# Kernel optimization log

Hardware: AMD Instinct MI355X
Metric: run time of the kernel (lower is better)

## Reference

```python
import jax, jax.numpy as jnp
import numpy as np

DIMS = 4

def mlp(x, W1, b1, W2, b2, W3, b3, Wo, bo):
    # x: (4,) -> scalar log(g_rr)
    h = jnp.tanh(x @ W1 + b1)
    h = jnp.tanh(h @ W2 + b2)
    h = jnp.tanh(h @ W3 + b3)
    return (h @ Wo + bo)[0]

def metric(x, params):
    # build_g: spherical metric with learned g_rr = exp(net(x))
    g_rr = jnp.exp(mlp(x, *params))
    r, th = x[1], x[2]
    diag = jnp.stack([-jnp.ones(()), g_rr, r ** 2, (r * jnp.sin(th)) ** 2])
    return jnp.diag(diag)  # (4,4)

def christoffel(x, params):
    g = metric(x, params)
    dg = jax.jacfwd(lambda xx: metric(xx, params))(x)  # dg[i,j,k] = d g_ij / d x^k
    g_inv = jnp.linalg.inv(g)
    # Gamma^a_bc = 0.5 g^{ad} (d_c g_db + d_b g_dc - d_d g_bc)
    sym = dg + jnp.transpose(dg, (0, 2, 1)) - jnp.transpose(dg, (2, 0, 1))
    gamma = 0.5 * jnp.einsum('ad,dbc->abc', g_inv, sym)
    return gamma, g_inv

def einstein_per_sample(x, params):
    gamma, g_inv = christoffel(x, params)
    # D[a,i,j,k] = d_k Gamma^a_ij (second nested forward-mode jacobian)
    D = jax.jacfwd(lambda xx: christoffel(xx, params)[0])(x)
    # R^a_bcd = d_c Gamma^a_db - d_d Gamma^a_cb + G^a_ce G^e_db - G^a_de G^e_cb
    riemann = (jnp.einsum('adbc->abcd', D) - jnp.einsum('acbd->abcd', D)
               + jnp.einsum('ace,edb->abcd', gamma, gamma)
               - jnp.einsum('ade,ecb->abcd', gamma, gamma))
    ricci = jnp.einsum('abad->bd', riemann)
    ricci_scalar = jnp.einsum('bd,bd->', g_inv, ricci)
    ricci_up = jnp.einsum('ac,bd,cd->ab', g_inv, g_inv, ricci)
    return ricci_up - 0.5 * g_inv * ricci_scalar  # contravariant Einstein tensor


def setup_inputs() -> dict:
    key = jax.random.key(0)
    ks = jax.random.split(key, 5)
    B, H = 8192, 256
    # coords in a well-conditioned region (avoid r ~ 0 which makes g singular)
    coords = jax.random.uniform(ks[0], (B, DIMS), dtype=jnp.float32) * 0.9 + 0.1
    def w(k, shape):
        fan_in = shape[0]
        return jax.random.normal(k, shape, dtype=jnp.float32) / np.sqrt(fan_in)
    return {
        'coords': coords,
        'W1': w(ks[1], (DIMS, H)), 'b1': jnp.zeros((H,), jnp.float32),
        'W2': w(ks[2], (H, H)),   'b2': jnp.zeros((H,), jnp.float32),
        'W3': w(ks[3], (H, H)),   'b3': jnp.zeros((H,), jnp.float32),
        'Wo': w(ks[4], (H, 1)),   'bo': jnp.zeros((1,), jnp.float32),
    }


def reference(coords, W1, b1, W2, b2, W3, b3, Wo, bo):
    params = (W1, b1, W2, b2, W3, b3, Wo, bo)
    # Batched Einstein tensor G^{ab}(x) for every sample: (B, 4, 4)
    return jax.vmap(lambda x: einstein_per_sample(x, params))(coords)
```

## Files before the change

### kernel.cpp

```cpp
#include <hip/hip_runtime.h>
#include <math.h>

typedef _Float16 half8 __attribute__((ext_vector_type(8)));
typedef float floatx4 __attribute__((ext_vector_type(4)));

#define HDIM 256
#define NC 15
#define NCP 16
#define SPB 8
#define MR 128
#define NWAVE 4
#define NT 4


__device__ __forceinline__ void einstein_tail(
    float f, const float* Gf, const float* Hs, float r, float th,
    float* __restrict__ outp)
{
    float Hf[4][4];
    {
        int qq = 0;
#pragma unroll
        for (int k = 0; k < 4; ++k)
#pragma unroll
            for (int l = k; l < 4; ++l) { Hf[k][l] = Hs[qq]; Hf[l][k] = Hs[qq]; ++qq; }
    }
    float sn = sinf(th), cs = cosf(th);
    float E  = expf(f);

    float gd[4] = {-1.f, E, r * r, r * r * sn * sn};
    float gi[4];
#pragma unroll
    for (int a = 0; a < 4; ++a) gi[a] = 1.f / gd[a];

    float dgv[4][4];
    float ddg[4][4][4];
#pragma unroll
    for (int a = 0; a < 4; ++a)
#pragma unroll
        for (int k = 0; k < 4; ++k) {
            dgv[a][k] = 0.f;
#pragma unroll
            for (int l = 0; l < 4; ++l) ddg[a][k][l] = 0.f;
        }
#pragma unroll
    for (int k = 0; k < 4; ++k) dgv[1][k] = E * Gf[k];
    dgv[2][1] = 2.f * r;
    dgv[3][1] = 2.f * r * sn * sn;
    dgv[3][2] = 2.f * r * r * sn * cs;
#pragma unroll
    for (int k = 0; k < 4; ++k)
#pragma unroll
        for (int l = 0; l < 4; ++l)
            ddg[1][k][l] = E * fmaf(Gf[k], Gf[l], Hf[k][l]);
    ddg[2][1][1] = 2.f;
    ddg[3][1][1] = 2.f * sn * sn;
    ddg[3][1][2] = 4.f * r * sn * cs;
    ddg[3][2][1] = 4.f * r * sn * cs;
    ddg[3][2][2] = 2.f * r * r * (cs * cs - sn * sn);

    auto SYMF = [&](int a, int i, int jx) -> float {
        float sy = 0.f;
        if (a == i)  sy += dgv[a][jx];
        if (a == jx) sy += dgv[a][i];
        if (i == jx) sy -= dgv[i][a];
        return sy;
    };
    auto DF = [&](int a, int i, int jx, int k) -> float {
        float ds = 0.f;
        if (a == i)  ds += ddg[a][jx][k];
        if (a == jx) ds += ddg[a][i][k];
        if (i == jx) ds -= ddg[i][a][k];
        return 0.5f * (gi[a] * ds - gi[a] * gi[a] * dgv[a][k] * SYMF(a, i, jx));
    };

    float Gm[4][4][4];
#pragma unroll
    for (int a = 0; a < 4; ++a)
#pragma unroll
        for (int i = 0; i < 4; ++i)
#pragma unroll
            for (int jx = 0; jx < 4; ++jx)
                Gm[a][i][jx] = 0.5f * gi[a] * SYMF(a, i, jx);

    float ric[4][4];
#pragma unroll
    for (int b = 0; b < 4; ++b)
#pragma unroll
        for (int d = 0; d < 4; ++d) {
            float sum = 0.f;
#pragma unroll
            for (int a = 0; a < 4; ++a) {
                sum += DF(a, d, b, a) - DF(a, a, b, d);
#pragma unroll
                for (int e = 0; e < 4; ++e)
                    sum += Gm[a][a][e] * Gm[e][d][b] - Gm[a][d][e] * Gm[e][a][b];
            }
            ric[b][d] = sum;
        }

    float Rs = 0.f;
#pragma unroll
    for (int b = 0; b < 4; ++b) Rs += gi[b] * ric[b][b];

#pragma unroll
    for (int a = 0; a < 4; ++a)
#pragma unroll
        for (int b = 0; b < 4; ++b) {
            float v = gi[a] * gi[b] * ric[a][b];
            if (a == b) v -= 0.5f * gi[a] * Rs;
            outp[a * 4 + b] = v;
        }
}

__global__ __launch_bounds__(256) void pack_wt(
    const float* __restrict__ W2, const float* __restrict__ W3,
    _Float16* __restrict__ Wt)
{
    __shared__ float t[64][65];
    const int m    = blockIdx.x >> 4;
    const float* W = m ? W3 : W2;
    const int tile = blockIdx.x & 15;
    const int k0 = (tile >> 2) * 64, j0 = (tile & 3) * 64;
    const int tx = threadIdx.x & 63, ty = threadIdx.x >> 6;
#pragma unroll
    for (int i = 0; i < 16; ++i) {
        int k = ty + i * 4;
        t[k][tx] = W[(k0 + k) * HDIM + j0 + tx];
    }
    __syncthreads();
#pragma unroll
    for (int i = 0; i < 16; ++i) {
        int jj = ty + i * 4;
        Wt[(size_t)m * HDIM * HDIM + (j0 + jj) * HDIM + k0 + tx] =
            (_Float16)t[tx][jj];
    }
}

template <bool TW>
__global__ __launch_bounds__(256, 2) void mlp_fused(
    const float* __restrict__ coords,
    const float* __restrict__ W1, const float* __restrict__ b1,
    const float* __restrict__ W2, const float* __restrict__ b2,
    const float* __restrict__ W3, const float* __restrict__ b3,
    const float* __restrict__ Wo, const float* __restrict__ bo,
    const _Float16* __restrict__ Wt,
    float* __restrict__ out, int B)
{
    __shared__ __align__(16) _Float16 st[MR * HDIM];

    const int tid  = threadIdx.x;
    const int w    = tid >> 6;
    const int lane = tid & 63;
    const int col  = lane & 15;
    const int q    = lane >> 4;
    const int s0   = blockIdx.x * SPB;

    floatx4 acc[8][NT];

    auto f4get = [](const float4& v, int i) -> float {
        switch (i & 3) { case 0: return v.x; case 1: return v.y;
                         case 2: return v.z; default: return v.w; }
    };

    auto produce1 = [&]() {
        const int sl = tid & 7;
        const int tc = tid >> 3;
        int ss = s0 + sl; if (ss >= B) ss = B - 1;
        const float x0 = coords[ss * 4 + 0];
        const float x1 = coords[ss * 4 + 1];
        const float x2 = coords[ss * 4 + 2];
        const float x3 = coords[ss * 4 + 3];
        const int jg = tc * 8;
        float4 wa[4][2];
#pragma unroll
        for (int k = 0; k < 4; ++k) {
            wa[k][0] = *(const float4*)&W1[k * HDIM + jg];
            wa[k][1] = *(const float4*)&W1[k * HDIM + jg + 4];
        }
        float4 bb0 = *(const float4*)&b1[jg];
        float4 bb1 = *(const float4*)&b1[jg + 4];
        half8 ch[NCP];
#pragma unroll
        for (int jj = 0; jj < 8; ++jj) ch[15][jj] = (_Float16)0.f;
#pragma unroll
        for (int jj = 0; jj < 8; ++jj) {
            const int h = jj >> 2;
            float w0 = f4get(wa[0][h], jj), w1 = f4get(wa[1][h], jj);
            float w2v = f4get(wa[2][h], jj), w3v = f4get(wa[3][h], jj);
            float a = f4get(h ? bb1 : bb0, jj);
            a = fmaf(x0, w0, a); a = fmaf(x1, w1, a);
            a = fmaf(x2, w2v, a); a = fmaf(x3, w3v, a);
            float v = tanhf(a), tp = 1.f - v * v, m2 = -2.f * v * tp;
            float g[4] = {w0, w1, w2v, w3v};
            ch[0][jj] = (_Float16)v;
#pragma unroll
            for (int k = 0; k < 4; ++k) ch[1 + k][jj] = (_Float16)(tp * g[k]);
            int idx = 5;
#pragma unroll
            for (int aa = 0; aa < 4; ++aa)
#pragma unroll
                for (int bb2 = aa; bb2 < 4; ++bb2) {
                    ch[idx][jj] = (_Float16)(m2 * g[aa] * g[bb2]); ++idx;
                }
        }
#pragma unroll
        for (int c = 0; c < NCP; ++c) {
            const int m = 16 * (c >> 1) + 4 * (sl >> 1) + 2 * (sl & 1) + (c & 1);
            const int addr = m * HDIM + (((tc ^ m) & 31) << 3);
            *(half8*)&st[addr] = ch[c];
        }
    };

    auto init_acc = [&](const float* __restrict__ b) {
#pragma unroll
        for (int nt = 0; nt < NT; ++nt) {
            float bj = b[w * 64 + nt * 16 + col];
#pragma unroll
            for (int mt = 0; mt < 8; ++mt)
#pragma unroll
                for (int r = 0; r < 4; ++r) acc[mt][nt][r] = 0.f;
            acc[0][nt][0] = bj;
            acc[0][nt][2] = bj;
        }
    };

    auto gemm_full = [&](const float* __restrict__ W, int layer) {
#pragma unroll
        for (int ks = 0; ks < 8; ++ks) {
            const int kg = ks * 32 + q * 8;
            half8 bf[NT];
#pragma unroll
            for (int nt = 0; nt < NT; ++nt) {
                const int j = w * 64 + nt * 16 + col;
                if constexpr (TW) {
                    bf[nt] = *(const half8*)&Wt[((size_t)layer * HDIM + j) * HDIM + kg];
                } else {
#pragma unroll
                    for (int i = 0; i < 8; ++i)
                        bf[nt][i] = (_Float16)W[(kg + i) * HDIM + j];
                }
            }
            const int lc = ks * 4 + q;
#pragma unroll
            for (int mt = 0; mt < 8; ++mt) {
                const int m = 16 * mt + col;
                half8 af = *(const half8*)&st[m * HDIM + (((lc ^ m) & 31) << 3)];
#pragma unroll
                for (int nt = 0; nt < NT; ++nt)
                    acc[mt][nt] = __builtin_amdgcn_mfma_f32_16x16x32_f16(
                        af, bf[nt], acc[mt][nt], 0, 0, 0);
            }
        }
    };

    auto transform_store = [&]() {
#pragma unroll
        for (int nt = 0; nt < NT; ++nt) {
            const int j = w * 64 + nt * 16 + col;
            const int jc = j >> 3, jb = j & 7;
#pragma unroll
            for (int sv = 0; sv < 2; ++sv) {
                float pre[NCP];
#pragma unroll
                for (int c = 0; c < NCP; ++c)
                    pre[c] = acc[c >> 1][nt][sv * 2 + (c & 1)];
                float v = tanhf(pre[0]), tp = 1.f - v * v, m2 = -2.f * v * tp;
                float g[4] = {pre[1], pre[2], pre[3], pre[4]};
                float ns[NCP];
                ns[0] = v;
#pragma unroll
                for (int k = 0; k < 4; ++k) ns[1 + k] = tp * g[k];
                int idx = 5;
#pragma unroll
                for (int aa = 0; aa < 4; ++aa)
#pragma unroll
                    for (int bb2 = aa; bb2 < 4; ++bb2) {
                        ns[idx] = fmaf(tp, pre[idx], m2 * g[aa] * g[bb2]); ++idx;
                    }
                ns[15] = 0.f;
#pragma unroll
                for (int c = 0; c < NCP; ++c) {
                    const int m = 16 * (c >> 1) + 4 * q + 2 * sv + (c & 1);
                    st[m * HDIM + (((jc ^ m) & 31) << 3) + jb] = (_Float16)ns[c];
                }
            }
        }
    };

    produce1();
    __syncthreads();
    init_acc(b2);
    gemm_full(W2, 0);
    __syncthreads();
    transform_store();
    __syncthreads();
    init_acc(b3);
    gemm_full(W3, 1);

    __syncthreads();
    float* part = (float*)st;
    float* fin  = ((float*)st) + 512;
    float wo[NT];
#pragma unroll
    for (int nt = 0; nt < NT; ++nt) wo[nt] = Wo[w * 64 + nt * 16 + col];

    float on2[2][NC];
#pragma unroll
    for (int sv = 0; sv < 2; ++sv)
#pragma unroll
        for (int c = 0; c < NC; ++c) on2[sv][c] = 0.f;
#pragma unroll
    for (int nt = 0; nt < NT; ++nt)
#pragma unroll
        for (int sv = 0; sv < 2; ++sv) {
            float pre[NCP];
#pragma unroll
            for (int c = 0; c < NCP; ++c)
                pre[c] = acc[c >> 1][nt][sv * 2 + (c & 1)];
            float v = tanhf(pre[0]), tp = 1.f - v * v, m2 = -2.f * v * tp;
            float g[4] = {pre[1], pre[2], pre[3], pre[4]};
            on2[sv][0] = fmaf(wo[nt], v, on2[sv][0]);
#pragma unroll
            for (int k = 0; k < 4; ++k)
                on2[sv][1 + k] = fmaf(wo[nt], tp * g[k], on2[sv][1 + k]);
            int idx = 5;
#pragma unroll
            for (int aa = 0; aa < 4; ++aa)
#pragma unroll
                for (int bb2 = aa; bb2 < 4; ++bb2) {
                    on2[sv][idx] = fmaf(wo[nt],
                        fmaf(tp, pre[idx], m2 * g[aa] * g[bb2]), on2[sv][idx]);
                    ++idx;
                }
        }
#pragma unroll
    for (int mask = 1; mask < 16; mask <<= 1)
#pragma unroll
        for (int sv = 0; sv < 2; ++sv)
#pragma unroll
            for (int c = 0; c < NC; ++c)
                on2[sv][c] += __shfl_xor(on2[sv][c], mask, 64);
    if (col == 0) {
#pragma unroll
        for (int sv = 0; sv < 2; ++sv)
#pragma unroll
            for (int c = 0; c < NC; ++c)
                part[(w * SPB + 2 * q + sv) * NC + c] = on2[sv][c];
    }
    __syncthreads();
    if (tid < SPB * NC) {
        const int sl = tid / NC, c = tid % NC;
        float v = 0.f;
#pragma unroll
        for (int ww = 0; ww < NWAVE; ++ww) v += part[(ww * SPB + sl) * NC + c];
        if (c == 0) v += bo[0];
        fin[sl * 16 + c] = v;
    }
    __syncthreads();
    if (tid < SPB) {
        int s = s0 + tid;
        if (s < B) {
            float f = fin[tid * 16 + 0];
            float Gf[4], Hs[10];
#pragma unroll
            for (int k = 0; k < 4; ++k) Gf[k] = fin[tid * 16 + 1 + k];
#pragma unroll
            for (int qq = 0; qq < 10; ++qq) Hs[qq] = fin[tid * 16 + 5 + qq];
            float r  = coords[s * 4 + 1];
            float th = coords[s * 4 + 2];
            float res[16];
            einstein_tail(f, Gf, Hs, r, th, res);
#pragma unroll
            for (int e = 0; e < 16; ++e) out[s * 16 + e] = res[e];
        }
    }
}

extern "C" void kernel_launch(void* const* d_in, const int* in_sizes, int n_in,
                              void* d_out, int out_size, void* d_ws, size_t ws_size,
                              hipStream_t stream) {
    const float* coords = (const float*)d_in[0];
    const float* W1 = (const float*)d_in[1];
    const float* b1 = (const float*)d_in[2];
    const float* W2 = (const float*)d_in[3];
    const float* b2 = (const float*)d_in[4];
    const float* W3 = (const float*)d_in[5];
    const float* b3 = (const float*)d_in[6];
    const float* Wo = (const float*)d_in[7];
    const float* bo = (const float*)d_in[8];
    float* out = (float*)d_out;
    const int B = in_sizes[0] / 4;
    const int nblocks = (B + SPB - 1) / SPB;

    const size_t wt_bytes = (size_t)2 * HDIM * HDIM * sizeof(_Float16);
    if (ws_size >= wt_bytes) {
        _Float16* Wt = (_Float16*)d_ws;
        pack_wt<<<32, 256, 0, stream>>>(W2, W3, Wt);
        mlp_fused<true><<<nblocks, 256, 0, stream>>>(
            coords, W1, b1, W2, b2, W3, b3, Wo, bo, Wt, out, B);
    } else {
        mlp_fused<false><<<nblocks, 256, 0, stream>>>(
            coords, W1, b1, W2, b2, W3, b3, Wo, bo, nullptr, out, B);
    }
}
```

Measured before the change: 133.6 us.

## Prefetch MFMA operands, use fast tanh, move Einstein tail to separate kernel

Double-buffers the weight fragments loaded from global memory and the activation fragments loaded from LDS inside the GEMM loop, so loads for the next k-step or m-tile are issued before the current MFMAs. Replaces tanhf with an exp-plus-reciprocal approximation. The per-sample Einstein tensor computation, previously run by only 8 threads per block after an extra barrier, moves into a separate kernel that reads the 15 MLP derivative values back from the output buffer and overwrites them in place. In exchange this adds a kernel launch and a round trip through global memory, raises register pressure from the prefetch buffers, and the fast tanh can lose accuracy or overflow for large inputs.

```diff
diff --git a/kernel.cpp b/kernel.cpp
--- a/kernel.cpp
+++ b/kernel.cpp
@@ -13,6 +13,11 @@
 #define NT 4
 
 
+__device__ __forceinline__ float ftanh(float x) {
+    float e = __expf(2.f * x);
+    return fmaf(-2.f, __builtin_amdgcn_rcpf(e + 1.f), 1.f);
+}
+
 __device__ __forceinline__ void einstein_tail(
     float f, const float* Gf, const float* Hs, float r, float th,
     float* __restrict__ outp)
@@ -111,6 +116,29 @@
             if (a == b) v -= 0.5f * gi[a] * Rs;
             outp[a * 4 + b] = v;
         }
+}
+
+__global__ __launch_bounds__(64) void einstein_k(
+    const float* __restrict__ coords, const float* __restrict__ bo,
+    float* io, int B)
+{
+    const int s = blockIdx.x * 64 + threadIdx.x;
+    if (s >= B) return;
+    float4 f0 = *(const float4*)&io[s * 16 + 0];
+    float4 f1 = *(const float4*)&io[s * 16 + 4];
+    float4 f2 = *(const float4*)&io[s * 16 + 8];
+    float4 f3 = *(const float4*)&io[s * 16 + 12];
+    float f = f0.x + bo[0];
+    float Gf[4] = {f0.y, f0.z, f0.w, f1.x};
+    float Hs[10] = {f1.y, f1.z, f1.w, f2.x, f2.y, f2.z, f2.w, f3.x, f3.y, f3.z};
+    float r  = coords[s * 4 + 1];
+    float th = coords[s * 4 + 2];
+    float res[16];
+    einstein_tail(f, Gf, Hs, r, th, res);
+#pragma unroll
+    for (int e = 0; e < 4; ++e)
+        *(float4*)&io[s * 16 + e * 4] =
+            make_float4(res[e*4+0], res[e*4+1], res[e*4+2], res[e*4+3]);
 }
 
 __global__ __launch_bounds__(256) void pack_wt(
@@ -143,7 +171,7 @@
     const float* __restrict__ W1, const float* __restrict__ b1,
     const float* __restrict__ W2, const float* __restrict__ b2,
     const float* __restrict__ W3, const float* __restrict__ b3,
-    const float* __restrict__ Wo, const float* __restrict__ bo,
+    const float* __restrict__ Wo,
     const _Float16* __restrict__ Wt,
     float* __restrict__ out, int B)
 {
@@ -191,7 +219,7 @@
             float a = f4get(h ? bb1 : bb0, jj);
             a = fmaf(x0, w0, a); a = fmaf(x1, w1, a);
             a = fmaf(x2, w2v, a); a = fmaf(x3, w3v, a);
-            float v = tanhf(a), tp = 1.f - v * v, m2 = -2.f * v * tp;
+            float v = ftanh(a), tp = 1.f - v * v, m2 = -2.f * v * tp;
             float g[4] = {w0, w1, w2v, w3v};
             ch[0][jj] = (_Float16)v;
 #pragma unroll
@@ -226,30 +254,52 @@
     };
 
     auto gemm_full = [&](const float* __restrict__ W, int layer) {
+        half8 bf[2][NT];
+#pragma unroll
+        for (int nt = 0; nt < NT; ++nt) {
+            const int j = w * 64 + nt * 16 + col;
+            if constexpr (TW) {
+                bf[0][nt] = *(const half8*)&Wt[((size_t)layer * HDIM + j) * HDIM + q * 8];
+            } else {
+#pragma unroll
+                for (int i = 0; i < 8; ++i)
+                    bf[0][nt][i] = (_Float16)W[(q * 8 + i) * HDIM + j];
+            }
+        }
 #pragma unroll
         for (int ks = 0; ks < 8; ++ks) {
-            const int kg = ks * 32 + q * 8;
-            half8 bf[NT];
-#pragma unroll
-            for (int nt = 0; nt < NT; ++nt) {
-                const int j = w * 64 + nt * 16 + col;
-                if constexpr (TW) {
-                    bf[nt] = *(const half8*)&Wt[((size_t)layer * HDIM + j) * HDIM + kg];
-                } else {
-#pragma unroll
-                    for (int i = 0; i < 8; ++i)
-                        bf[nt][i] = (_Float16)W[(kg + i) * HDIM + j];
+            const int cur = ks & 1, nxt = cur ^ 1;
+            if (ks < 7) {
+                const int kg2 = (ks + 1) * 32 + q * 8;
+#pragma unroll
+                for (int nt = 0; nt < NT; ++nt) {
+                    const int j = w * 64 + nt * 16 + col;
+                    if constexpr (TW) {
+                        bf[nxt][nt] = *(const half8*)&Wt[((size_t)layer * HDIM + j) * HDIM + kg2];
+                    } else {
+#pragma unroll
+                        for (int i = 0; i < 8; ++i)
+                            bf[nxt][nt][i] = (_Float16)W[(kg2 + i) * HDIM + j];
+                    }
                 }
             }
             const int lc = ks * 4 + q;
+            half8 af[2];
+            {
+                const int m0 = col;
+                af[0] = *(const half8*)&st[m0 * HDIM + (((lc ^ m0) & 31) << 3)];
+            }
 #pragma unroll
             for (int mt = 0; mt < 8; ++mt) {
-                const int m = 16 * mt + col;
-                half8 af = *(const half8*)&st[m * HDIM + (((lc ^ m) & 31) << 3)];
+                if (mt < 7) {
+                    const int m1 = 16 * (mt + 1) + col;
+                    af[(mt + 1) & 1] =
+                        *(const half8*)&st[m1 * HDIM + (((lc ^ m1) & 31) << 3)];
+                }
 #pragma unroll
                 for (int nt = 0; nt < NT; ++nt)
                     acc[mt][nt] = __builtin_amdgcn_mfma_f32_16x16x32_f16(
-                        af, bf[nt], acc[mt][nt], 0, 0, 0);
+                        af[mt & 1], bf[cur][nt], acc[mt][nt], 0, 0, 0);
             }
         }
     };
@@ -265,7 +315,7 @@
 #pragma unroll
                 for (int c = 0; c < NCP; ++c)
                     pre[c] = acc[c >> 1][nt][sv * 2 + (c & 1)];
-                float v = tanhf(pre[0]), tp = 1.f - v * v, m2 = -2.f * v * tp;
+                float v = ftanh(pre[0]), tp = 1.f - v * v, m2 = -2.f * v * tp;
                 float g[4] = {pre[1], pre[2], pre[3], pre[4]};
                 float ns[NCP];
                 ns[0] = v;
@@ -300,7 +350,6 @@
 
     __syncthreads();
     float* part = (float*)st;
-    float* fin  = ((float*)st) + 512;
     float wo[NT];
 #pragma unroll
     for (int nt = 0; nt < NT; ++nt) wo[nt] = Wo[w * 64 + nt * 16 + col];
@@ -318,7 +367,7 @@
 #pragma unroll
             for (int c = 0; c < NCP; ++c)
                 pre[c] = acc[c >> 1][nt][sv * 2 + (c & 1)];
-            float v = tanhf(pre[0]), tp = 1.f - v * v, m2 = -2.f * v * tp;
+            float v = ftanh(pre[0]), tp = 1.f - v * v, m2 = -2.f * v * tp;
             float g[4] = {pre[1], pre[2], pre[3], pre[4]};
             on2[sv][0] = fmaf(wo[nt], v, on2[sv][0]);
 #pragma unroll
@@ -354,26 +403,8 @@
         float v = 0.f;
 #pragma unroll
         for (int ww = 0; ww < NWAVE; ++ww) v += part[(ww * SPB + sl) * NC + c];
-        if (c == 0) v += bo[0];
-        fin[sl * 16 + c] = v;
-    }
-    __syncthreads();
-    if (tid < SPB) {
-        int s = s0 + tid;
-        if (s < B) {
-            float f = fin[tid * 16 + 0];
-            float Gf[4], Hs[10];
-#pragma unroll
-            for (int k = 0; k < 4; ++k) Gf[k] = fin[tid * 16 + 1 + k];
-#pragma unroll
-            for (int qq = 0; qq < 10; ++qq) Hs[qq] = fin[tid * 16 + 5 + qq];
-            float r  = coords[s * 4 + 1];
-            float th = coords[s * 4 + 2];
-            float res[16];
-            einstein_tail(f, Gf, Hs, r, th, res);
-#pragma unroll
-            for (int e = 0; e < 16; ++e) out[s * 16 + e] = res[e];
-        }
+        int s = s0 + sl;
+        if (s < B) out[s * 16 + c] = v;
     }
 }
 
@@ -398,9 +429,10 @@
         _Float16* Wt = (_Float16*)d_ws;
         pack_wt<<<32, 256, 0, stream>>>(W2, W3, Wt);
         mlp_fused<true><<<nblocks, 256, 0, stream>>>(
-            coords, W1, b1, W2, b2, W3, b3, Wo, bo, Wt, out, B);
+            coords, W1, b1, W2, b2, W3, b3, Wo, Wt, out, B);
     } else {
         mlp_fused<false><<<nblocks, 256, 0, stream>>>(
-            coords, W1, b1, W2, b2, W3, b3, Wo, bo, nullptr, out, B);
-    }
-}
+            coords, W1, b1, W2, b2, W3, b3, Wo, nullptr, out, B);
+    }
+    einstein_k<<<(B + 63) / 64, 64, 0, stream>>>(coords, bo, out, B);
+}
```

Measured after the change: 123.9 us. -7.3%, faster.
